# Kernel tuning notes

Hardware: AMD Instinct MI355X
Metric: run time of the kernel (lower is better)

Reference implementation:

```python
import jax, jax.numpy as jnp
import numpy as np

B, T, D, H = 2, 512, 512, 8
HD = D // H
FF = 4 * D
MOM_BETA, NOV_BETA, NOV_GAIN = 0.9, 0.95, 3.0
LR_MIN, LR_MAX, MAX_FW_NORM = 0.5, 3.0, 32.0


def setup_inputs() -> dict:
    key = jax.random.key(0)
    ks = jax.random.split(key, 10)
    s = 1.0 / np.sqrt(D)
    return {
        'x': jax.random.normal(ks[0], (B, T, D), jnp.float32),
        'Wq': jax.random.normal(ks[1], (D, D), jnp.float32) * s,
        'Wk1': jax.random.normal(ks[2], (D, D), jnp.float32) * s,
        'Wk2': jax.random.normal(ks[3], (D, D), jnp.float32) * s,
        'Wv': jax.random.normal(ks[4], (D, D), jnp.float32) * s,
        'Wo': jax.random.normal(ks[5], (D, D), jnp.float32) * s,
        'lambda_logit': jnp.zeros((H,), jnp.float32),  # sigmoid -> lambda_init = 0.5
        'ln1_g': jnp.ones((D,), jnp.float32), 'ln1_b': jnp.zeros((D,), jnp.float32),
        'base_weight': jax.random.normal(ks[6], (D, D), jnp.float32) * s,  # ~xavier
        'ttt_bias': jnp.zeros((D,), jnp.float32),
        'log_inner_lr': jnp.log(jnp.asarray(0.05, jnp.float32)),
        'ln2_g': jnp.ones((D,), jnp.float32), 'ln2_b': jnp.zeros((D,), jnp.float32),
        'W1': jax.random.normal(ks[7], (FF, D), jnp.float32) * s,
        'b1': jnp.zeros((FF,), jnp.float32),
        'W2': jax.random.normal(ks[8], (D, FF), jnp.float32) * (1.0 / np.sqrt(FF)),
        'b2': jnp.zeros((D,), jnp.float32),
        'ln3_g': jnp.ones((D,), jnp.float32), 'ln3_b': jnp.zeros((D,), jnp.float32),
    }


def _ln(x, g, b):
    m = x.mean(-1, keepdims=True)
    v = jnp.mean((x - m) ** 2, -1, keepdims=True)
    return (x - m) / jnp.sqrt(v + 1e-5) * g + b


def _diff_attn(x, Wq, Wk1, Wk2, Wv, Wo, lambda_logit):
    b, t, d = x.shape
    def heads(w):
        return jnp.einsum('btd,od->bto', x, w).reshape(b, t, H, HD).transpose(0, 2, 1, 3)
    q, k1, k2, v = heads(Wq), heads(Wk1), heads(Wk2), heads(Wv)
    scale = HD ** -0.5
    s1 = jnp.einsum('bhqd,bhkd->bhqk', q, k1) * scale
    s2 = jnp.einsum('bhqd,bhkd->bhqk', q, k2) * scale
    mask = jnp.tril(jnp.ones((t, t), bool))
    neg = jnp.finfo(s1.dtype).min
    s1 = jnp.where(mask, s1, neg)
    s2 = jnp.where(mask, s2, neg)
    lam = jax.nn.sigmoid(lambda_logit)[None, :, None, None]
    attn = jax.nn.softmax(s1, -1) - lam * jax.nn.softmax(s2, -1)
    attn = attn / jnp.clip(jnp.abs(attn).sum(-1, keepdims=True), 1e-6, None)
    o = jnp.einsum('bhqk,bhkd->bhqd', attn, v).transpose(0, 2, 1, 3).reshape(b, t, d)
    return jnp.einsum('btd,od->bto', o, Wo)


def _ttt(x, base_weight, ttt_bias, log_inner_lr):
    b = x.shape[0]
    inner_lr = jnp.clip(jnp.exp(log_inner_lr), 1e-5, 1.0)
    fw0 = jnp.broadcast_to(base_weight, (b, D, D)).astype(x.dtype) + 0.0
    mom0 = jnp.zeros_like(fw0)
    ema0 = jnp.zeros((b, D), x.dtype)
    lrm0 = jnp.ones((b, 1), x.dtype)

    def step(carry, x_t):  # x_t: [B, D]
        fw, mom, ema, lrm = carry
        y = jnp.einsum('bij,bj->bi', fw, x_t) + ttt_bias
        err = (y - x_t) / float(D)  # targets=None -> target is x_t
        g = jax.lax.stop_gradient(err[:, :, None] * x_t[:, None, :])  # first_order
        mom2 = MOM_BETA * mom + (1.0 - MOM_BETA) * g
        nov = jnp.abs(x_t - ema).mean(-1, keepdims=True)  # [B, 1]
        lr_scale = jnp.clip(1.0 + NOV_GAIN * nov, LR_MIN, LR_MAX)
        lrm2 = NOV_BETA * lrm + (1.0 - NOV_BETA) * lr_scale
        ema2 = NOV_BETA * ema + (1.0 - NOV_BETA) * x_t
        fw2 = fw - (inner_lr * lrm2)[:, :, None] * mom2
        norm = jnp.clip(jnp.sqrt((fw2 * fw2).sum((1, 2), keepdims=True)), 1e-6, None)
        fw2 = fw2 * jnp.minimum(MAX_FW_NORM / norm, 1.0)
        return (fw2, mom2, ema2, lrm2), y

    _, ys = jax.lax.scan(step, (fw0, mom0, ema0, lrm0), x.transpose(1, 0, 2))
    return ys.transpose(1, 0, 2)


def reference(x, Wq, Wk1, Wk2, Wv, Wo, lambda_logit, ln1_g, ln1_b, base_weight, ttt_bias, log_inner_lr, ln2_g, ln2_b, W1, b1, W2, b2, ln3_g, ln3_b):
    h = x + _diff_attn(_ln(x, ln1_g, ln1_b), Wq, Wk1, Wk2, Wv, Wo, lambda_logit)
    h = h + _ttt(_ln(h, ln2_g, ln2_b), base_weight, ttt_bias, log_inner_lr)
    z = _ln(h, ln3_g, ln3_b)
    z = jax.nn.gelu(jnp.einsum('btd,fd->btf', z, W1) + b1, approximate=False)
    h = h + jnp.einsum('btf,df->btd', z, W2) + b2
    return h
```

## Files before the change

kernel.cpp:

```cpp
#include <hip/hip_runtime.h>
#include <hip/hip_fp16.h>

typedef _Float16 f16;
typedef f16 f16x4 __attribute__((ext_vector_type(4)));
typedef f16 f16x8 __attribute__((ext_vector_type(8)));
typedef float f32x4 __attribute__((ext_vector_type(4)));
typedef unsigned uint2v __attribute__((ext_vector_type(2)));

#define DEVI static __device__ __forceinline__

DEVI void gload_lds16(const void* g, void* l) {
  __builtin_amdgcn_global_load_lds(
      (const __attribute__((address_space(1))) unsigned int*)g,
      (__attribute__((address_space(3))) unsigned int*)l, 16, 0, 0);
}

DEVI float wave_red_sum64(float v) {
#pragma unroll
  for (int m = 1; m < 64; m <<= 1) v += __shfl_xor(v, m, 64);
  return v;
}
DEVI float wave_red_max64(float v) {
#pragma unroll
  for (int m = 1; m < 64; m <<= 1) v = fmaxf(v, __shfl_xor(v, m, 64));
  return v;
}

template <int CTRL>
DEVI float dpp_addf(float v) {
  int s = __builtin_amdgcn_update_dpp(0, __float_as_int(v), CTRL, 0xF, 0xF, true);
  return v + __int_as_float(s);
}
DEVI float xor16_add(float v) {
#if __has_builtin(__builtin_amdgcn_permlane16_swap)
  uint2v r = __builtin_amdgcn_permlane16_swap(__float_as_uint(v), __float_as_uint(v), false, false);
  return __uint_as_float(r.x) + __uint_as_float(r.y);
#else
  int s = __builtin_amdgcn_ds_swizzle(__float_as_int(v), 0x401F);
  return v + __int_as_float(s);
#endif
}
DEVI float xor32_add(float v) {
#if __has_builtin(__builtin_amdgcn_permlane32_swap)
  uint2v r = __builtin_amdgcn_permlane32_swap(__float_as_uint(v), __float_as_uint(v), false, false);
  return __uint_as_float(r.x) + __uint_as_float(r.y);
#else
  int s = __builtin_amdgcn_ds_bpermute(((threadIdx.x & 63) ^ 32) << 2, __float_as_int(v));
  return v + __int_as_float(s);
#endif
}
DEVI float allred64(float v) {
  v = dpp_addf<0xB1>(v);
  v = dpp_addf<0x4E>(v);
  v = dpp_addf<0x141>(v);
  v = dpp_addf<0x140>(v);
  v = xor16_add(v);
  return xor32_add(v);
}
DEVI float red16g(float v) {
  v = dpp_addf<0xB1>(v);
  v = dpp_addf<0x4E>(v);
  v = dpp_addf<0x141>(v);
  v = dpp_addf<0x140>(v);
  return v;
}

__global__ void cvt_all_kernel(const float* __restrict__ s0, const float* __restrict__ s1,
                               const float* __restrict__ s2, const float* __restrict__ s3,
                               const float* __restrict__ s4, const float* __restrict__ s5,
                               const float* __restrict__ s6, f16* __restrict__ d) {
  const int blk = blockIdx.x;
  const float* s; long dofs; int local;
  if (blk < 256)       { s = s0; dofs = 0;       local = blk; }
  else if (blk < 512)  { s = s1; dofs = 262144;  local = blk - 256; }
  else if (blk < 768)  { s = s2; dofs = 524288;  local = blk - 512; }
  else if (blk < 1024) { s = s3; dofs = 786432;  local = blk - 768; }
  else if (blk < 1280) { s = s4; dofs = 1048576; local = blk - 1024; }
  else if (blk < 2304) { s = s5; dofs = 1310720; local = blk - 1280; }
  else                 { s = s6; dofs = 2359296; local = blk - 2304; }
  const long i = (long)local * 1024 + threadIdx.x * 4;
  float4 v = *(const float4*)(s + i);
  f16x4 o = {(f16)v.x, (f16)v.y, (f16)v.z, (f16)v.w};
  *(f16x4*)(d + dofs + i) = o;
}

__global__ void ln_kernel(const float* __restrict__ in, const float* __restrict__ add,
                          const float* __restrict__ g, const float* __restrict__ b,
                          float* __restrict__ sumout, float* __restrict__ lnf,
                          f16* __restrict__ lnh) {
  const int row = blockIdx.x * 4 + (threadIdx.x >> 6);
  const int lane = threadIdx.x & 63;
  const long base = (long)row * 512;
  const int c0 = lane * 4, c1 = 256 + lane * 4;
  float4 a0 = *(const float4*)(in + base + c0);
  float4 a1 = *(const float4*)(in + base + c1);
  if (add) {
    float4 d0 = *(const float4*)(add + base + c0);
    float4 d1 = *(const float4*)(add + base + c1);
    a0.x += d0.x; a0.y += d0.y; a0.z += d0.z; a0.w += d0.w;
    a1.x += d1.x; a1.y += d1.y; a1.z += d1.z; a1.w += d1.w;
  }
  if (sumout) {
    *(float4*)(sumout + base + c0) = a0;
    *(float4*)(sumout + base + c1) = a1;
  }
  float v[8] = {a0.x, a0.y, a0.z, a0.w, a1.x, a1.y, a1.z, a1.w};
  float s = 0.f;
#pragma unroll
  for (int k = 0; k < 8; k++) s += v[k];
  s = wave_red_sum64(s);
  const float mean = s * (1.f / 512.f);
  float vs = 0.f;
#pragma unroll
  for (int k = 0; k < 8; k++) { float d = v[k] - mean; vs += d * d; }
  vs = wave_red_sum64(vs);
  const float rstd = rsqrtf(vs * (1.f / 512.f) + 1e-5f);
  float4 g0 = *(const float4*)(g + c0), g1 = *(const float4*)(g + c1);
  float4 p0 = *(const float4*)(b + c0), p1 = *(const float4*)(b + c1);
  const float gg[8] = {g0.x, g0.y, g0.z, g0.w, g1.x, g1.y, g1.z, g1.w};
  const float bv[8] = {p0.x, p0.y, p0.z, p0.w, p1.x, p1.y, p1.z, p1.w};
  float y[8];
#pragma unroll
  for (int k = 0; k < 8; k++) y[k] = (v[k] - mean) * rstd * gg[k] + bv[k];
  if (lnf) {
    float4 o0 = {y[0], y[1], y[2], y[3]}, o1 = {y[4], y[5], y[6], y[7]};
    *(float4*)(lnf + base + c0) = o0;
    *(float4*)(lnf + base + c1) = o1;
  }
  if (lnh) {
    f16x4 o0 = {(f16)y[0], (f16)y[1], (f16)y[2], (f16)y[3]};
    f16x4 o1 = {(f16)y[4], (f16)y[5], (f16)y[6], (f16)y[7]};
    *(f16x4*)(lnh + base + c0) = o0;
    *(f16x4*)(lnh + base + c1) = o1;
  }
}

enum { EPI_QKV = 0, EPI_SCORES = 2, EPI_PV = 3, EPI_GELU = 5, EPI_PART = 7 };

template <int EPI>
__launch_bounds__(256, 1) __global__
void gemm_bt(const f16* __restrict__ A, const f16* __restrict__ W, int lda, int ldw,
             long Az, long Wz, void* __restrict__ dst, const float* __restrict__ bias,
             const float* __restrict__ resid, int K, float scale, int zofs, int hcp) {
  if (EPI == EPI_SCORES && blockIdx.x > blockIdx.y) return;
  __shared__ f16 lA[128 * 64];
  __shared__ f16 lB[128 * 64];
  const int tid = threadIdx.x;
  const int wave = tid >> 6, lane = tid & 63;
  const int z = blockIdx.z;
  const f16* Ab;
  const f16* Wb;
  if (EPI == EPI_SCORES) {
    const int v_ = (z >= hcp) ? 1 : 0, head = z - v_ * hcp;
    Ab = A + (long)head * 32768 + (long)blockIdx.y * 128 * lda;
    Wb = W + (long)v_ * 524288 + (long)head * 32768 + (long)blockIdx.x * 128 * ldw;
  } else {
    Ab = A + (long)z * Az + (long)blockIdx.y * 128 * lda;
    Wb = W + (long)z * Wz + (long)blockIdx.x * 128 * ldw;
  }

  f32x4 acc[4][4];
#pragma unroll
  for (int a = 0; a < 4; a++)
#pragma unroll
    for (int q = 0; q < 4; q++) acc[a][q] = (f32x4){0.f, 0.f, 0.f, 0.f};

  int srow[4], scol[4];
#pragma unroll
  for (int i = 0; i < 4; i++) {
    int c = i * 256 + tid;
    int row = c >> 3;
    int colb = (c & 7) << 4;
    srow[i] = row;
    scol[i] = (colb ^ ((row & 7) << 4)) >> 1;
  }

  for (int k0 = 0; k0 < K; k0 += 64) {
    __syncthreads();
#pragma unroll
    for (int i = 0; i < 4; i++) {
      const int le = (i * 256 + wave * 64) * 8;
      gload_lds16(Ab + (long)srow[i] * lda + k0 + scol[i], lA + le);
      gload_lds16(Wb + (long)srow[i] * ldw + k0 + scol[i], lB + le);
    }
    __syncthreads();
    const int wm = (wave >> 1) * 64, wn = (wave & 1) * 64;
#pragma unroll
    for (int km = 0; km < 2; km++) {
      const int kb = km * 64 + ((lane >> 4) << 4);
      f16x8 af[4], bfv[4];
#pragma unroll
      for (int mf = 0; mf < 4; mf++) {
        int r = wm + mf * 16 + (lane & 15);
        af[mf] = *(const f16x8*)((const char*)lA + r * 128 + (kb ^ ((r & 7) << 4)));
      }
#pragma unroll
      for (int nf = 0; nf < 4; nf++) {
        int r = wn + nf * 16 + (lane & 15);
        bfv[nf] = *(const f16x8*)((const char*)lB + r * 128 + (kb ^ ((r & 7) << 4)));
      }
#pragma unroll
      for (int mf = 0; mf < 4; mf++)
#pragma unroll
        for (int nf = 0; nf < 4; nf++)
          acc[mf][nf] = __builtin_amdgcn_mfma_f32_16x16x32_f16(af[mf], bfv[nf], acc[mf][nf], 0, 0, 0);
    }
  }

  const int wm = (wave >> 1) * 64, wn = (wave & 1) * 64;
  const int rbase = blockIdx.y * 128 + wm + ((lane >> 4) << 2);
  const int cbase = blockIdx.x * 128 + wn + (lane & 15);
#pragma unroll
  for (int mf = 0; mf < 4; mf++)
#pragma unroll
    for (int nf = 0; nf < 4; nf++)
#pragma unroll
      for (int j = 0; j < 4; j++) {
        const int m = rbase + mf * 16 + j;
        const int n = cbase + nf * 16;
        const float v = acc[mf][nf][j];
        if (EPI == EPI_QKV) {
          f16* d = (f16*)dst + (long)z * 524288;
          if (z < 3)
            d[(long)((m >> 9) * 8 + (n >> 6)) * 32768 + (m & 511) * 64 + (n & 63)] = (f16)v;
          else
            d[(long)((m >> 9) * 8 + (n >> 6)) * 32768 + (n & 63) * 512 + (m & 511)] = (f16)v;
        } else if (EPI == EPI_SCORES) {
          ((float*)dst)[(long)z * 262144 + (long)m * 512 + n] = v * scale;
        } else if (EPI == EPI_PV) {
          if (n < 64) {
            const int hh = z + zofs;
            ((f16*)dst)[(long)((hh >> 3) * 512 + m) * 512 + (hh & 7) * 64 + n] = (f16)v;
          }
        } else if (EPI == EPI_GELU) {
          const float u = v + bias[n];
          ((f16*)dst)[(long)m * 2048 + n] = (f16)(0.5f * u * (1.f + erff(u * 0.70710678118f)));
        } else {
          ((float*)dst)[(long)z * 524288 + (long)m * 512 + n] = v;
        }
      }
}

__global__ void red4_kernel(const float* __restrict__ parts, const float* __restrict__ resid,
                            const float* __restrict__ bias, float* __restrict__ dst) {
  const long i = ((long)blockIdx.x * 256 + threadIdx.x) * 4;
  float4 s0 = *(const float4*)(parts + i);
  float4 s1 = *(const float4*)(parts + 524288 + i);
  float4 s2 = *(const float4*)(parts + 1048576 + i);
  float4 s3 = *(const float4*)(parts + 1572864 + i);
  float4 r  = *(const float4*)(resid + i);
  float4 o;
  o.x = ((s0.x + s1.x) + (s2.x + s3.x)) + r.x;
  o.y = ((s0.y + s1.y) + (s2.y + s3.y)) + r.y;
  o.z = ((s0.z + s1.z) + (s2.z + s3.z)) + r.z;
  o.w = ((s0.w + s1.w) + (s2.w + s3.w)) + r.w;
  if (bias) {
    const int n = (int)(i & 511);
    float4 b = *(const float4*)(bias + n);
    o.x += b.x; o.y += b.y; o.z += b.z; o.w += b.w;
  }
  *(float4*)(dst + i) = o;
}

__global__ void softmax_diff_kernel(const float* __restrict__ S1, const float* __restrict__ S2,
                                    const float* __restrict__ lamlog, f16* __restrict__ attn,
                                    int zofs) {
  const int rid = blockIdx.x * 4 + (threadIdx.x >> 6);
  const int lane = threadIdx.x & 63;
  const int z = rid >> 9, i = rid & 511;
  const float lam = 1.f / (1.f + __expf(-lamlog[(z + zofs) & 7]));
  const long base = (long)z * 262144 + (long)i * 512;
  const int c0 = lane * 4, c1 = 256 + lane * 4;
  float4 xa = *(const float4*)(S1 + base + c0);
  float4 xb = *(const float4*)(S1 + base + c1);
  float4 ya = *(const float4*)(S2 + base + c0);
  float4 yb = *(const float4*)(S2 + base + c1);
  float s1v[8] = {xa.x, xa.y, xa.z, xa.w, xb.x, xb.y, xb.z, xb.w};
  float s2v[8] = {ya.x, ya.y, ya.z, ya.w, yb.x, yb.y, yb.z, yb.w};
  int cols[8];
#pragma unroll
  for (int k = 0; k < 8; k++) cols[k] = (k < 4) ? (c0 + k) : (c1 + k - 4);
  float m1 = -3.0e38f, m2 = -3.0e38f;
#pragma unroll
  for (int k = 0; k < 8; k++)
    if (cols[k] <= i) { m1 = fmaxf(m1, s1v[k]); m2 = fmaxf(m2, s2v[k]); }
  m1 = wave_red_max64(m1);
  m2 = wave_red_max64(m2);
  float z1 = 0.f, z2 = 0.f, e1[8], e2[8];
#pragma unroll
  for (int k = 0; k < 8; k++) {
    const bool valid = cols[k] <= i;
    e1[k] = valid ? __expf(s1v[k] - m1) : 0.f;
    e2[k] = valid ? __expf(s2v[k] - m2) : 0.f;
    z1 += e1[k]; z2 += e2[k];
  }
  z1 = wave_red_sum64(z1);
  z2 = wave_red_sum64(z2);
  const float r1 = 1.f / z1, r2 = lam / z2;
  float p[8], l1 = 0.f;
#pragma unroll
  for (int k = 0; k < 8; k++) { p[k] = e1[k] * r1 - e2[k] * r2; l1 += fabsf(p[k]); }
  l1 = wave_red_sum64(l1);
  const float rn = 1.f / fmaxf(l1, 1e-6f);
  f16x4 o0 = {(f16)(p[0] * rn), (f16)(p[1] * rn), (f16)(p[2] * rn), (f16)(p[3] * rn)};
  f16x4 o1 = {(f16)(p[4] * rn), (f16)(p[5] * rn), (f16)(p[6] * rn), (f16)(p[7] * rn)};
  *(f16x4*)(attn + base + c0) = o0;
  *(f16x4*)(attn + base + c1) = o1;
}

#define ALD4(dst, p) asm volatile("global_load_dwordx4 %0, %1, off" : "=&v"(dst) : "v"(p) : "memory")
#define ALD1(dst, p) asm volatile("global_load_dword %0, %1, off" : "=&v"(dst) : "v"(p) : "memory")
#define VMWAIT(N)                                                             \
  {                                                                           \
    asm volatile("s_waitcnt vmcnt(" #N ")" ::: "memory");                     \
    __builtin_amdgcn_sched_barrier(0);                                        \
  }

#define EISSUE(X)                                                             \
  {                                                                           \
    ALD1(X[0], pe);        ALD1(X[1], pe + 512);                              \
    ALD1(X[2], pe + 1024); ALD1(X[3], pe + 1536);                             \
    ALD1(X[4], pe + 2048); ALD1(X[5], pe + 2560);                             \
    ALD1(X[6], pe + 3072); ALD1(X[7], pe + 3584);                             \
    pe += 4096;                                                               \
  }
#define ESTEP(V, T)                                                           \
  {                                                                           \
    dp[(long)(T) * 512] = fabsf((V) - ema);                                   \
    ema = fmaf(0.95f, ema, 0.05f * (V));                                      \
  }

__launch_bounds__(64, 1) __global__
void eta_diff_kernel(const float* __restrict__ x2, float* __restrict__ diff) {
  const int blk = blockIdx.x;
  const int b = blk >> 3;
  const int col = (blk & 7) * 64 + threadIdx.x;
  const float* pe = x2 + (long)b * 262144 + col;
  float* dp = diff + (long)b * 262144 + col;
  float ema = 0.f;
  float EA[8], EB[8];
  EISSUE(EA);
  EISSUE(EB);
  VMWAIT(8);
#pragma unroll 1
  for (int t = 0; t < 512; t += 16) {
    ESTEP(EA[0], t + 0); ESTEP(EA[1], t + 1); ESTEP(EA[2], t + 2); ESTEP(EA[3], t + 3);
    ESTEP(EA[4], t + 4); ESTEP(EA[5], t + 5); ESTEP(EA[6], t + 6); ESTEP(EA[7], t + 7);
    EISSUE(EA);
    VMWAIT(16);
    ESTEP(EB[0], t + 8);  ESTEP(EB[1], t + 9);  ESTEP(EB[2], t + 10); ESTEP(EB[3], t + 11);
    ESTEP(EB[4], t + 12); ESTEP(EB[5], t + 13); ESTEP(EB[6], t + 14); ESTEP(EB[7], t + 15);
    EISSUE(EB);
    VMWAIT(16);
  }
  asm volatile("s_waitcnt vmcnt(0)" ::: "memory");
}

__global__ void eta_nov_kernel(const float* __restrict__ diff, float* __restrict__ nov) {
  const int row = blockIdx.x * 4 + (threadIdx.x >> 6);
  const int lane = threadIdx.x & 63;
  const float* dp = diff + (long)row * 512 + lane * 4;
  float4 a0 = *(const float4*)dp;
  float4 a1 = *(const float4*)(dp + 256);
  float s = ((a0.x + a0.y) + (a0.z + a0.w)) + ((a1.x + a1.y) + (a1.z + a1.w));
  s = wave_red_sum64(s);
  if (lane == 0) nov[row] = s * (1.f / 512.f);
}

__global__ void eta_scan_kernel(const float* __restrict__ nov, const float* __restrict__ loglr,
                                float* __restrict__ eta) {
  if (threadIdx.x != 0) return;
  const int b = blockIdx.x;
  float ilr = expf(loglr[0]);
  ilr = fminf(fmaxf(ilr, 1e-5f), 1.f);
  float lrm = 1.f;
  const float* pb = nov + (long)b * 512;
#pragma unroll 8
  for (int t = 0; t < 512; t++) {
    const float ls = fminf(fmaxf(fmaf(3.f, pb[t], 1.f), 0.5f), 3.f);
    lrm = fmaf(0.95f, lrm, 0.05f * ls);
    eta[b * 512 + t] = ilr * lrm;
  }
}

DEVI float dot8(const f32x4 F0, const f32x4 F1, const f32x4 X0, const f32x4 X1) {
  float a0 = F0.x * X0.x, a1 = F0.y * X0.y, a2 = F0.z * X0.z, a3 = F0.w * X0.w;
  a0 = fmaf(F1.x, X1.x, a0); a1 = fmaf(F1.y, X1.y, a1);
  a2 = fmaf(F1.z, X1.z, a2); a3 = fmaf(F1.w, X1.w, a3);
  return (a0 + a1) + (a2 + a3);
}
DEVI void upd8(f32x4& M0, f32x4& M1, f32x4& F0, f32x4& F1, float c1, float e,
               const f32x4 X0, const f32x4 X1, float& ns) {
  M0.x = fmaf(0.9f, M0.x, c1 * X0.x); F0.x = fmaf(-e, M0.x, F0.x); ns = fmaf(F0.x, F0.x, ns);
  M0.y = fmaf(0.9f, M0.y, c1 * X0.y); F0.y = fmaf(-e, M0.y, F0.y); ns = fmaf(F0.y, F0.y, ns);
  M0.z = fmaf(0.9f, M0.z, c1 * X0.z); F0.z = fmaf(-e, M0.z, F0.z); ns = fmaf(F0.z, F0.z, ns);
  M0.w = fmaf(0.9f, M0.w, c1 * X0.w); F0.w = fmaf(-e, M0.w, F0.w); ns = fmaf(F0.w, F0.w, ns);
  M1.x = fmaf(0.9f, M1.x, c1 * X1.x); F1.x = fmaf(-e, M1.x, F1.x); ns = fmaf(F1.x, F1.x, ns);
  M1.y = fmaf(0.9f, M1.y, c1 * X1.y); F1.y = fmaf(-e, M1.y, F1.y); ns = fmaf(F1.y, F1.y, ns);
  M1.z = fmaf(0.9f, M1.z, c1 * X1.z); F1.z = fmaf(-e, M1.z, F1.z); ns = fmaf(F1.z, F1.z, ns);
  M1.w = fmaf(0.9f, M1.w, c1 * X1.w); F1.w = fmaf(-e, M1.w, F1.w); ns = fmaf(F1.w, F1.w, ns);
}

#define TISSUE2(X, RA, RB, ET)                                                \
  {                                                                           \
    ALD4(X[0], pxc);        ALD4(X[1], pxc + 4);                              \
    ALD4(X[2], pxc + 512);  ALD4(X[3], pxc + 516);                            \
    ALD4(X[4], pxc + 1024); ALD4(X[5], pxc + 1028);                           \
    ALD4(X[6], pxc + 1536); ALD4(X[7], pxc + 1540);                           \
    ALD1(RA[0], pxra);        ALD1(RA[1], pxra + 512);                        \
    ALD1(RA[2], pxra + 1024); ALD1(RA[3], pxra + 1536);                       \
    ALD1(RB[0], pxrb);        ALD1(RB[1], pxrb + 512);                        \
    ALD1(RB[2], pxrb + 1024); ALD1(RB[3], pxrb + 1536);                       \
    ALD4(ET, per);                                                            \
    pxc += 2048; pxra += 2048; pxrb += 2048; per += 4;                        \
  }

#define TSTEP2(X0v, X1v, rAv, rBv, ev, K)                                     \
  {                                                                           \
    const float pA_ = allred64(dot8(fA0, fA1, X0v, X1v));                     \
    const float pB_ = allred64(dot8(fB0, fB1, X0v, X1v));                     \
    const float yA_ = pA_ + biasA, yB_ = pB_ + biasB;                         \
    ysA[K] = yA_; ysB[K] = yB_;                                               \
    const float c1A_ = (yA_ - (rAv)) * (0.1f / 512.f);                        \
    const float c1B_ = (yB_ - (rBv)) * (0.1f / 512.f);                        \
    const float e_ = (ev);                                                    \
    float ns_ = 0.f;                                                          \
    upd8(mA0, mA1, fA0, fA1, c1A_, e_, X0v, X1v, ns_);                        \
    upd8(mB0, mB1, fB0, fB1, c1B_, e_, X0v, X1v, ns_);                        \
    np8[K] = allred64(ns_);                                                   \
  }

__launch_bounds__(64, 1) __global__
void ttt_fast_kernel(const float* __restrict__ x2, const float* __restrict__ base_w,
                     const float* __restrict__ tbias, const float* __restrict__ eta,
                     float* __restrict__ yT, float* __restrict__ npT) {
  const int blk = blockIdx.x;
  const int b = blk >> 8;
  const int rA = blk & 255;
  const int lane = threadIdx.x;
  const float* xb = x2 + (long)b * 262144;

  f32x4 fA0, fA1, fB0, fB1;
  float biasA, biasB;
  ALD4(fA0, base_w + (long)rA * 512 + lane * 8);
  ALD4(fA1, base_w + (long)rA * 512 + lane * 8 + 4);
  ALD4(fB0, base_w + (long)(rA + 256) * 512 + lane * 8);
  ALD4(fB1, base_w + (long)(rA + 256) * 512 + lane * 8 + 4);
  ALD1(biasA, tbias + rA);
  ALD1(biasB, tbias + rA + 256);

  f32x4 mA0 = {0.f, 0.f, 0.f, 0.f}, mA1 = mA0, mB0 = mA0, mB1 = mA0;
  float ysA[8], ysB[8], np8[8];

  const float* pxc = xb + lane * 8;
  const float* pxra = xb + rA;
  const float* pxrb = xb + rA + 256;
  const float* per = eta + b * 512;
  float* pyA = yT + (long)(b * 512 + rA) * 512;
  float* pyB = yT + (long)(b * 512 + rA + 256) * 512;
  float* pnp = npT + (long)blk * 512;

  f32x4 XA[8], XB[8], EA, EB;
  float RA0[4], RB0[4], RA1[4], RB1[4];
  TISSUE2(XA, RA0, RB0, EA);
  TISSUE2(XB, RA1, RB1, EB);
  VMWAIT(17);

#pragma unroll 1
  for (int T = 0; T < 512; T += 8) {
    TSTEP2(XA[0], XA[1], RA0[0], RB0[0], EA.x, 0);
    TSTEP2(XA[2], XA[3], RA0[1], RB0[1], EA.y, 1);
    TSTEP2(XA[4], XA[5], RA0[2], RB0[2], EA.z, 2);
    TSTEP2(XA[6], XA[7], RA0[3], RB0[3], EA.w, 3);
    TISSUE2(XA, RA0, RB0, EA);
    VMWAIT(17);
    TSTEP2(XB[0], XB[1], RA1[0], RB1[0], EB.x, 4);
    TSTEP2(XB[2], XB[3], RA1[1], RB1[1], EB.y, 5);
    TSTEP2(XB[4], XB[5], RA1[2], RB1[2], EB.z, 6);
    TSTEP2(XB[6], XB[7], RA1[3], RB1[3], EB.w, 7);
    if (lane == 0) {
      *(float4*)(pyA + T)     = (float4){ysA[0], ysA[1], ysA[2], ysA[3]};
      *(float4*)(pyA + T + 4) = (float4){ysA[4], ysA[5], ysA[6], ysA[7]};
      *(float4*)(pyB + T)     = (float4){ysB[0], ysB[1], ysB[2], ysB[3]};
      *(float4*)(pyB + T + 4) = (float4){ysB[4], ysB[5], ysB[6], ysB[7]};
      *(float4*)(pnp + T)     = (float4){np8[0], np8[1], np8[2], np8[3]};
      *(float4*)(pnp + T + 4) = (float4){np8[4], np8[5], np8[6], np8[7]};
    }
    TISSUE2(XB, RA1, RB1, EB);
    VMWAIT(23);
  }
  asm volatile("s_waitcnt vmcnt(0)" ::: "memory");
}

__global__ void transpose3_kernel(const float* __restrict__ yT, const float* __restrict__ npT,
                                  float* __restrict__ ysb, float* __restrict__ npv) {
  __shared__ float tile[64][65];
  const int s = blockIdx.z;
  const float* src = (s < 2) ? (yT + (long)s * 262144) : npT;
  float* dst = (s < 2) ? (ysb + (long)s * 262144) : npv;
  const int ti = blockIdx.y, tj = blockIdx.x;
  const int tr = threadIdx.x >> 4;
  const int tc = (threadIdx.x & 15) * 4;
#pragma unroll
  for (int p = 0; p < 4; p++) {
    const int r = tr + p * 16;
    float4 v = *(const float4*)(src + (long)(ti * 64 + r) * 512 + tj * 64 + tc);
    tile[r][tc] = v.x; tile[r][tc + 1] = v.y; tile[r][tc + 2] = v.z; tile[r][tc + 3] = v.w;
  }
  __syncthreads();
#pragma unroll
  for (int p = 0; p < 4; p++) {
    const int j = tr + p * 16;
    float4 v = {tile[tc][j], tile[tc + 1][j], tile[tc + 2][j], tile[tc + 3][j]};
    *(float4*)(dst + (long)(tj * 64 + j) * 512 + ti * 64 + tc) = v;
  }
}

__global__ void verify_kernel(const float* __restrict__ npv, int* __restrict__ flag) {
  const int t = blockIdx.x;
  const int tid = threadIdx.x;
  const int wave = tid >> 6, lane = tid & 63;
  float s = npv[(long)t * 512 + tid];
  s = wave_red_sum64(s);
  __shared__ float part[8];
  if (lane == 0) part[wave] = s;
  __syncthreads();
  if (tid == 0) {
    const float s0 = (part[0] + part[1]) + (part[2] + part[3]);
    const float s1 = (part[4] + part[5]) + (part[6] + part[7]);
    if (s0 > 1020.f || s1 > 1020.f) atomicOr(flag, 1);
  }
}

__launch_bounds__(1024, 1) __global__
void ttt_fallback_kernel(const int* __restrict__ flag, const float* __restrict__ x2,
                         const float* __restrict__ base_w, const float* __restrict__ tbias,
                         const float* __restrict__ eta, float* __restrict__ ys,
                         float* __restrict__ fwg, float* __restrict__ momg) {
  if (flag[0] == 0) return;
  const int b = blockIdx.x;
  const int tid = threadIdx.x;
  const int wave = tid >> 6, lane = tid & 63;
  float* fw = fwg + (long)b * 262144;
  float* mm = momg + (long)b * 262144;
  for (int e = tid; e < 262144; e += 1024) { fw[e] = base_w[e]; mm[e] = 0.f; }
  __shared__ float xs[512], errs[512], red[16];
  const float* xb = x2 + (long)b * 262144;
  for (int t = 0; t < 512; t++) {
    __syncthreads();
    if (tid < 512) xs[tid] = xb[t * 512 + tid];
    __syncthreads();
    if (tid < 512) {
      float acc = 0.f;
      for (int c = 0; c < 512; c++) acc = fmaf(fw[(long)tid * 512 + c], xs[c], acc);
      const float y = acc + tbias[tid];
      ys[((long)b * 512 + t) * 512 + tid] = y;
      errs[tid] = (y - xs[tid]) * (1.f / 512.f);
    }
    __syncthreads();
    const float eta_t = eta[b * 512 + t];
    float nsq = 0.f;
    for (int e = tid; e < 262144; e += 1024) {
      const int r = e >> 9, c = e & 511;
      const float m2 = fmaf(0.9f, mm[e], 0.1f * errs[r] * xs[c]);
      mm[e] = m2;
      const float f2 = fmaf(-eta_t, m2, fw[e]);
      fw[e] = f2;
      nsq = fmaf(f2, f2, nsq);
    }
    nsq = wave_red_sum64(nsq);
    if (lane == 0) red[wave] = nsq;
    __syncthreads();
    if (tid == 0) {
      float s = 0.f;
      for (int w = 0; w < 16; w++) s += red[w];
      red[0] = s;
    }
    __syncthreads();
    const float norm = fmaxf(sqrtf(red[0]), 1e-6f);
    const float sc = fminf(32.f / norm, 1.f);
    if (sc < 1.f)
      for (int e = tid; e < 262144; e += 1024) fw[e] *= sc;
  }
}

extern "C" void kernel_launch(void* const* d_in, const int* in_sizes, int n_in,
                              void* d_out, int out_size, void* d_ws, size_t ws_size,
                              hipStream_t stream) {
  (void)in_sizes; (void)n_in; (void)out_size;
  const float* x      = (const float*)d_in[0];
  const float* Wq     = (const float*)d_in[1];
  const float* Wk1    = (const float*)d_in[2];
  const float* Wk2    = (const float*)d_in[3];
  const float* Wv     = (const float*)d_in[4];
  const float* Wo     = (const float*)d_in[5];
  const float* lamlog = (const float*)d_in[6];
  const float* ln1g   = (const float*)d_in[7];
  const float* ln1b   = (const float*)d_in[8];
  const float* basew  = (const float*)d_in[9];
  const float* tttb   = (const float*)d_in[10];
  const float* loglr  = (const float*)d_in[11];
  const float* ln2g   = (const float*)d_in[12];
  const float* ln2b   = (const float*)d_in[13];
  const float* W1     = (const float*)d_in[14];
  const float* b1     = (const float*)d_in[15];
  const float* W2     = (const float*)d_in[16];
  const float* b2     = (const float*)d_in[17];
  const float* ln3g   = (const float*)d_in[18];
  const float* ln3b   = (const float*)d_in[19];
  float* out = (float*)d_out;

  char* ws = (char*)d_ws;
  size_t off = 0;
  auto alloc = [&](size_t bytes) {
    size_t o = off;
    off += (bytes + 255) & ~(size_t)255;
    return o;
  };
  f16* WqH   = (f16*)(ws + alloc(262144 * 2));
  f16* Wk1H  = (f16*)(ws + alloc(262144 * 2));
  f16* Wk2H  = (f16*)(ws + alloc(262144 * 2));
  f16* WvH   = (f16*)(ws + alloc(262144 * 2));
  f16* WoH   = (f16*)(ws + alloc(262144 * 2));
  f16* W1H   = (f16*)(ws + alloc(1048576 * 2));
  f16* W2H   = (f16*)(ws + alloc(1048576 * 2));
  (void)Wk1H; (void)Wk2H; (void)WvH; (void)W1H;
  f16* xlnH  = (f16*)(ws + alloc(524288 * 2));
  f16* qh    = (f16*)(ws + alloc(524288 * 2));
  f16* k1h   = (f16*)(ws + alloc(524288 * 2));
  f16* k2h   = (f16*)(ws + alloc(524288 * 2));
  f16* vTh   = (f16*)(ws + alloc(524288 * 2));
  (void)k2h;
  f16* obtd  = (f16*)(ws + alloc(524288 * 2));
  f16* x3h   = (f16*)(ws + alloc(524288 * 2));
  f16* zh    = (f16*)(ws + alloc(2097152 * 2));
  float* h1  = (float*)(ws + alloc(524288 * 4));
  float* x2  = (float*)(ws + alloc(524288 * 4));
  float* ysb = (float*)(ws + alloc(524288 * 4));
  float* h2  = (float*)(ws + alloc(524288 * 4));
  float* eta = (float*)(ws + alloc(1024 * 4));
  float* yT  = (float*)(ws + alloc(524288 * 4));
  float* npT = (float*)(ws + alloc(262144 * 4));
  float* npv = (float*)(ws + alloc(262144 * 4));
  float* nvd = (float*)(ws + alloc(524288 * 4));
  float* nov = (float*)(ws + alloc(1024 * 4));
  int* flag  = (int*)(ws + alloc(256));
  float* fwfb  = (float*)(ws + alloc(524288 * 4));
  float* momfb = (float*)(ws + alloc(524288 * 4));
  float* parts = (float*)(ws + alloc((size_t)4 * 524288 * 4));

  int hc = 16;
  while (hc > 1 && off + (size_t)hc * (262144ull * 4 * 2 + 262144ull * 2) > ws_size) hc >>= 1;
  float* S1  = (float*)(ws + alloc((size_t)hc * 262144 * 4));
  float* S2  = (float*)(ws + alloc((size_t)hc * 262144 * 4));
  f16* attnb = (f16*)(ws + alloc((size_t)hc * 262144 * 2));
  (void)S2;

  cvt_all_kernel<<<3328, 256, 0, stream>>>(Wq, Wk1, Wk2, Wv, Wo, W1, W2, WqH);

  ln_kernel<<<256, 256, 0, stream>>>(x, nullptr, ln1g, ln1b, nullptr, nullptr, xlnH);

  gemm_bt<EPI_QKV><<<dim3(4, 8, 4), 256, 0, stream>>>(
      xlnH, WqH, 512, 512, 0, 262144, qh, nullptr, nullptr, 512, 1.f, 0, 0);

  const int nc = 16 / hc;
  for (int c = 0; c < nc; c++) {
    const int cs = c * hc;
    gemm_bt<EPI_SCORES><<<dim3(4, 4, 2 * hc), 256, 0, stream>>>(
        qh + (long)cs * 32768, k1h + (long)cs * 32768, 64, 64, 0, 0, S1,
        nullptr, nullptr, 64, 0.125f, 0, hc);
    softmax_diff_kernel<<<hc * 128, 256, 0, stream>>>(S1, S2, lamlog, attnb, cs);
    gemm_bt<EPI_PV><<<dim3(1, 4, hc), 256, 0, stream>>>(
        attnb, vTh + (long)cs * 32768, 512, 512, 262144, 32768, obtd,
        nullptr, nullptr, 512, 1.f, cs, 0);
  }

  gemm_bt<EPI_PART><<<dim3(4, 8, 4), 256, 0, stream>>>(
      obtd, WoH, 512, 512, 128, 128, parts, nullptr, nullptr, 128, 1.f, 0, 0);
  red4_kernel<<<512, 256, 0, stream>>>(parts, x, nullptr, h1);

  ln_kernel<<<256, 256, 0, stream>>>(h1, nullptr, ln2g, ln2b, nullptr, x2, nullptr);

  hipMemsetAsync(flag, 0, 4, stream);
  eta_diff_kernel<<<16, 64, 0, stream>>>(x2, nvd);
  eta_nov_kernel<<<256, 256, 0, stream>>>(nvd, nov);
  eta_scan_kernel<<<2, 64, 0, stream>>>(nov, loglr, eta);
  ttt_fast_kernel<<<512, 64, 0, stream>>>(x2, basew, tttb, eta, yT, npT);
  transpose3_kernel<<<dim3(8, 8, 3), 256, 0, stream>>>(yT, npT, ysb, npv);
  verify_kernel<<<512, 512, 0, stream>>>(npv, flag);
  ttt_fallback_kernel<<<2, 1024, 0, stream>>>(flag, x2, basew, tttb, eta, ysb, fwfb, momfb);

  ln_kernel<<<256, 256, 0, stream>>>(h1, ysb, ln3g, ln3b, h2, nullptr, x3h);

  gemm_bt<EPI_GELU><<<dim3(16, 8, 1), 256, 0, stream>>>(x3h, W1H, 512, 512, 0, 0, zh, b1, nullptr, 512, 1.f, 0, 0);
  gemm_bt<EPI_PART><<<dim3(4, 8, 4), 256, 0, stream>>>(
      zh, W2H, 2048, 2048, 512, 512, parts, nullptr, nullptr, 512, 1.f, 0, 0);
  red4_kernel<<<512, 256, 0, stream>>>(parts, h2, b2, out);
}
```

Baseline: 290.9 us.

## Replace per-step norm reduction with running max and cheaper wave reduction in TTT

The TTT scan kernel no longer reduces and stores the per-step squared norm across the whole wave. Each lane now keeps a running maximum of its partial norm, which is reduced once at the end to a single per-block bound. The per-step norm buffer, its transpose slice and the 512-block verify pass shrink to one value per block and a single-block verify. The dot-product reduction uses DPP row broadcasts plus a readlane instead of permlane swaps. In exchange the fallback check becomes a conservative bound with a lowered threshold, which may trigger the fallback path in cases the exact check did not.

```diff
diff --git a/kernel.cpp b/kernel.cpp
--- a/kernel.cpp
+++ b/kernel.cpp
@@ -5,7 +5,6 @@
 typedef f16 f16x4 __attribute__((ext_vector_type(4)));
 typedef f16 f16x8 __attribute__((ext_vector_type(8)));
 typedef float f32x4 __attribute__((ext_vector_type(4)));
-typedef unsigned uint2v __attribute__((ext_vector_type(2)));
 
 #define DEVI static __device__ __forceinline__
 
@@ -31,38 +30,16 @@
   int s = __builtin_amdgcn_update_dpp(0, __float_as_int(v), CTRL, 0xF, 0xF, true);
   return v + __int_as_float(s);
 }
-DEVI float xor16_add(float v) {
-#if __has_builtin(__builtin_amdgcn_permlane16_swap)
-  uint2v r = __builtin_amdgcn_permlane16_swap(__float_as_uint(v), __float_as_uint(v), false, false);
-  return __uint_as_float(r.x) + __uint_as_float(r.y);
-#else
-  int s = __builtin_amdgcn_ds_swizzle(__float_as_int(v), 0x401F);
-  return v + __int_as_float(s);
-#endif
-}
-DEVI float xor32_add(float v) {
-#if __has_builtin(__builtin_amdgcn_permlane32_swap)
-  uint2v r = __builtin_amdgcn_permlane32_swap(__float_as_uint(v), __float_as_uint(v), false, false);
-  return __uint_as_float(r.x) + __uint_as_float(r.y);
-#else
-  int s = __builtin_amdgcn_ds_bpermute(((threadIdx.x & 63) ^ 32) << 2, __float_as_int(v));
-  return v + __int_as_float(s);
-#endif
-}
-DEVI float allred64(float v) {
+DEVI float redsum64(float v) {
   v = dpp_addf<0xB1>(v);
   v = dpp_addf<0x4E>(v);
   v = dpp_addf<0x141>(v);
   v = dpp_addf<0x140>(v);
-  v = xor16_add(v);
-  return xor32_add(v);
-}
-DEVI float red16g(float v) {
-  v = dpp_addf<0xB1>(v);
-  v = dpp_addf<0x4E>(v);
-  v = dpp_addf<0x141>(v);
-  v = dpp_addf<0x140>(v);
-  return v;
+  int t = __builtin_amdgcn_update_dpp(0, __float_as_int(v), 0x142, 0xA, 0xF, true);
+  v += __int_as_float(t);
+  t = __builtin_amdgcn_update_dpp(0, __float_as_int(v), 0x143, 0xC, 0xF, true);
+  v += __int_as_float(t);
+  return __int_as_float(__builtin_amdgcn_readlane(__float_as_int(v), 63));
 }
 
 __global__ void cvt_all_kernel(const float* __restrict__ s0, const float* __restrict__ s1,
@@ -417,8 +394,8 @@
 
 #define TSTEP2(X0v, X1v, rAv, rBv, ev, K)                                     \
   {                                                                           \
-    const float pA_ = allred64(dot8(fA0, fA1, X0v, X1v));                     \
-    const float pB_ = allred64(dot8(fB0, fB1, X0v, X1v));                     \
+    const float pA_ = redsum64(dot8(fA0, fA1, X0v, X1v));                     \
+    const float pB_ = redsum64(dot8(fB0, fB1, X0v, X1v));                     \
     const float yA_ = pA_ + biasA, yB_ = pB_ + biasB;                         \
     ysA[K] = yA_; ysB[K] = yB_;                                               \
     const float c1A_ = (yA_ - (rAv)) * (0.1f / 512.f);                        \
@@ -427,13 +404,13 @@
     float ns_ = 0.f;                                                          \
     upd8(mA0, mA1, fA0, fA1, c1A_, e_, X0v, X1v, ns_);                        \
     upd8(mB0, mB1, fB0, fB1, c1B_, e_, X0v, X1v, ns_);                        \
-    np8[K] = allred64(ns_);                                                   \
+    nsmax = fmaxf(nsmax, ns_);                                                \
   }
 
 __launch_bounds__(64, 1) __global__
 void ttt_fast_kernel(const float* __restrict__ x2, const float* __restrict__ base_w,
                      const float* __restrict__ tbias, const float* __restrict__ eta,
-                     float* __restrict__ yT, float* __restrict__ npT) {
+                     float* __restrict__ yT, float* __restrict__ npB) {
   const int blk = blockIdx.x;
   const int b = blk >> 8;
   const int rA = blk & 255;
@@ -450,7 +427,8 @@
   ALD1(biasB, tbias + rA + 256);
 
   f32x4 mA0 = {0.f, 0.f, 0.f, 0.f}, mA1 = mA0, mB0 = mA0, mB1 = mA0;
-  float ysA[8], ysB[8], np8[8];
+  float ysA[8], ysB[8];
+  float nsmax = 0.f;
 
   const float* pxc = xb + lane * 8;
   const float* pxra = xb + rA;
@@ -458,7 +436,6 @@
   const float* per = eta + b * 512;
   float* pyA = yT + (long)(b * 512 + rA) * 512;
   float* pyB = yT + (long)(b * 512 + rA + 256) * 512;
-  float* pnp = npT + (long)blk * 512;
 
   f32x4 XA[8], XB[8], EA, EB;
   float RA0[4], RB0[4], RA1[4], RB1[4];
@@ -483,21 +460,20 @@
       *(float4*)(pyA + T + 4) = (float4){ysA[4], ysA[5], ysA[6], ysA[7]};
       *(float4*)(pyB + T)     = (float4){ysB[0], ysB[1], ysB[2], ysB[3]};
       *(float4*)(pyB + T + 4) = (float4){ysB[4], ysB[5], ysB[6], ysB[7]};
-      *(float4*)(pnp + T)     = (float4){np8[0], np8[1], np8[2], np8[3]};
-      *(float4*)(pnp + T + 4) = (float4){np8[4], np8[5], np8[6], np8[7]};
     }
     TISSUE2(XB, RA1, RB1, EB);
-    VMWAIT(23);
+    VMWAIT(21);
   }
   asm volatile("s_waitcnt vmcnt(0)" ::: "memory");
-}
-
-__global__ void transpose3_kernel(const float* __restrict__ yT, const float* __restrict__ npT,
-                                  float* __restrict__ ysb, float* __restrict__ npv) {
+  const float tot = redsum64(nsmax);
+  if (lane == 0) npB[blk] = tot;
+}
+
+__global__ void transpose2_kernel(const float* __restrict__ yT, float* __restrict__ ysb) {
   __shared__ float tile[64][65];
   const int s = blockIdx.z;
-  const float* src = (s < 2) ? (yT + (long)s * 262144) : npT;
-  float* dst = (s < 2) ? (ysb + (long)s * 262144) : npv;
+  const float* src = yT + (long)s * 262144;
+  float* dst = ysb + (long)s * 262144;
   const int ti = blockIdx.y, tj = blockIdx.x;
   const int tr = threadIdx.x >> 4;
   const int tc = (threadIdx.x & 15) * 4;
@@ -516,19 +492,17 @@
   }
 }
 
-__global__ void verify_kernel(const float* __restrict__ npv, int* __restrict__ flag) {
-  const int t = blockIdx.x;
+__global__ void verify_kernel(const float* __restrict__ npB, int* __restrict__ flag) {
   const int tid = threadIdx.x;
   const int wave = tid >> 6, lane = tid & 63;
-  float s = npv[(long)t * 512 + tid];
-  s = wave_red_sum64(s);
+  float s = wave_red_sum64(npB[tid]);
   __shared__ float part[8];
   if (lane == 0) part[wave] = s;
   __syncthreads();
   if (tid == 0) {
     const float s0 = (part[0] + part[1]) + (part[2] + part[3]);
     const float s1 = (part[4] + part[5]) + (part[6] + part[7]);
-    if (s0 > 1020.f || s1 > 1020.f) atomicOr(flag, 1);
+    if (s0 > 1000.f || s1 > 1000.f) atomicOr(flag, 1);
   }
 }
 
@@ -640,8 +614,7 @@
   float* h2  = (float*)(ws + alloc(524288 * 4));
   float* eta = (float*)(ws + alloc(1024 * 4));
   float* yT  = (float*)(ws + alloc(524288 * 4));
-  float* npT = (float*)(ws + alloc(262144 * 4));
-  float* npv = (float*)(ws + alloc(262144 * 4));
+  float* npB = (float*)(ws + alloc(512 * 4));
   float* nvd = (float*)(ws + alloc(524288 * 4));
   float* nov = (float*)(ws + alloc(1024 * 4));
   int* flag  = (int*)(ws + alloc(256));
@@ -685,9 +658,9 @@
   eta_diff_kernel<<<16, 64, 0, stream>>>(x2, nvd);
   eta_nov_kernel<<<256, 256, 0, stream>>>(nvd, nov);
   eta_scan_kernel<<<2, 64, 0, stream>>>(nov, loglr, eta);
-  ttt_fast_kernel<<<512, 64, 0, stream>>>(x2, basew, tttb, eta, yT, npT);
-  transpose3_kernel<<<dim3(8, 8, 3), 256, 0, stream>>>(yT, npT, ysb, npv);
-  verify_kernel<<<512, 512, 0, stream>>>(npv, flag);
+  ttt_fast_kernel<<<512, 64, 0, stream>>>(x2, basew, tttb, eta, yT, npB);
+  transpose2_kernel<<<dim3(8, 8, 2), 256, 0, stream>>>(yT, ysb);
+  verify_kernel<<<1, 512, 0, stream>>>(npB, flag);
   ttt_fallback_kernel<<<2, 1024, 0, stream>>>(flag, x2, basew, tttb, eta, ysb, fwfb, momfb);
 
   ln_kernel<<<256, 256, 0, stream>>>(h1, ysb, ln3g, ln3b, h2, nullptr, x3h);
```

Result: faster. 283.3 us (-2.6%).
